# Kernel optimization log

Measured on AMD Instinct MI355X. Metric: run time of the kernel, lower is better.

The kernel has to match this reference:

```python
import jax, jax.numpy as jnp
import numpy as np

BOUND = 1.0          # aabb = [-bound, bound]^3 (aabb_train/aabb_infer)
MIN_NEAR = 0.2
DENSITY_SCALE = 1.0
T_THRESH = 1e-4
BG_COLOR = 1.0
N_RAYS = 262144      # 512x512 image
N_STEPS = 128        # samples per ray


def setup_inputs() -> dict:
    key = jax.random.key(0)
    k1, k2, k3, k4 = jax.random.split(key, 4)
    # ray origins inside the box, unit directions
    rays_o = jax.random.uniform(k1, (N_RAYS, 3), minval=-0.5, maxval=0.5)
    d = jax.random.normal(k2, (N_RAYS, 3))
    rays_d = d / jnp.linalg.norm(d, axis=-1, keepdims=True)
    # per-sample network outputs (the abstract self(xyzs, dirs) call)
    sigmas = jax.random.uniform(k3, (N_RAYS, N_STEPS)) * 10.0
    rgbs = jax.random.uniform(k4, (N_RAYS, N_STEPS, 3))
    return {"rays_o": rays_o, "rays_d": rays_d, "sigmas": sigmas, "rgbs": rgbs}


def reference(rays_o, rays_d, sigmas, rgbs):
    N, S = sigmas.shape
    # --- near_far_from_aabb: slab test against [-BOUND, BOUND]^3 ---
    d = jnp.where(jnp.abs(rays_d) < 1e-8, 1e-8, rays_d)
    t1 = (-BOUND - rays_o) / d                      # [N,3]
    t2 = (BOUND - rays_o) / d                       # [N,3]
    nears = jnp.max(jnp.minimum(t1, t2), axis=-1)   # [N]
    fars = jnp.min(jnp.maximum(t1, t2), axis=-1)    # [N]
    nears = jnp.maximum(nears, MIN_NEAR)
    fars = jnp.maximum(fars, nears + 1e-4)

    # --- uniform marching: per-ray step size ---
    deltas = (fars - nears) / S                     # [N]
    tvals = nears[:, None] + (jnp.arange(S, dtype=sigmas.dtype) + 0.5) * deltas[:, None]  # [N,S]

    # --- composite_rays: alpha compositing with early-termination mask ---
    alphas = 1.0 - jnp.exp(-DENSITY_SCALE * sigmas * deltas[:, None])       # [N,S]
    trans_full = jnp.cumprod(1.0 - alphas + 1e-10, axis=1)                   # [N,S]
    # exclusive transmittance: T_i = prod_{j<i} (1 - alpha_j)
    T = jnp.concatenate([jnp.ones_like(trans_full[:, :1]), trans_full[:, :-1]], axis=1)
    # the CUDA kernel stops marching once T < T_thresh
    weights = alphas * T * (T > T_THRESH).astype(sigmas.dtype)               # [N,S]

    weights_sum = jnp.sum(weights, axis=1)                                   # [N]
    depth = jnp.sum(weights * tvals, axis=1)                                 # [N]
    image = jnp.einsum('ns,nsc->nc', weights, rgbs)                          # [N,3]
    image = image + (1.0 - weights_sum)[:, None] * BG_COLOR
    depth_normalized = jnp.clip(depth - nears, 0.0) / (fars - nears)
    return image, depth, depth_normalized
```

## Files before the change

kernel.cpp:

```cpp
#include <hip/hip_runtime.h>

#define NSTEPS 128
#define MIN_NEAR 0.2f
#define T_THRESH 1e-4f

__global__ __launch_bounds__(256) void nerf_composite(
    const float* __restrict__ rays_o,
    const float* __restrict__ rays_d,
    const float* __restrict__ sigmas,
    const float* __restrict__ rgbs,
    float* __restrict__ out,
    int N)
{
    const int ray  = blockIdx.x * 4 + (threadIdx.x >> 6);
    const int lane = threadIdx.x & 63;
    if (ray >= N) return;

    const float o0 = rays_o[3 * ray + 0];
    const float o1 = rays_o[3 * ray + 1];
    const float o2 = rays_o[3 * ray + 2];
    const float d0 = rays_d[3 * ray + 0];
    const float d1 = rays_d[3 * ray + 1];
    const float d2 = rays_d[3 * ray + 2];

    float tmin = -3.0e38f, tmax = 3.0e38f;
    {
        float dc, ta, tb;
        dc = (fabsf(d0) < 1e-8f) ? 1e-8f : d0;
        ta = (-1.0f - o0) / dc;  tb = (1.0f - o0) / dc;
        tmin = fmaxf(tmin, fminf(ta, tb));  tmax = fminf(tmax, fmaxf(ta, tb));
        dc = (fabsf(d1) < 1e-8f) ? 1e-8f : d1;
        ta = (-1.0f - o1) / dc;  tb = (1.0f - o1) / dc;
        tmin = fmaxf(tmin, fminf(ta, tb));  tmax = fminf(tmax, fmaxf(ta, tb));
        dc = (fabsf(d2) < 1e-8f) ? 1e-8f : d2;
        ta = (-1.0f - o2) / dc;  tb = (1.0f - o2) / dc;
        tmin = fmaxf(tmin, fminf(ta, tb));  tmax = fminf(tmax, fmaxf(ta, tb));
    }
    const float nearv = fmaxf(tmin, MIN_NEAR);
    const float farv  = fmaxf(tmax, nearv + 1e-4f);
    const float delta = (farv - nearv) * (1.0f / (float)NSTEPS);

    const float2* sp = (const float2*)(sigmas + (size_t)ray * NSTEPS);
    const float2 sv = sp[lane];
    const float2* rp = (const float2*)(rgbs + (size_t)ray * NSTEPS * 3);
    const float2 c0 = rp[3 * lane + 0];
    const float2 c1 = rp[3 * lane + 1];
    const float2 c2 = rp[3 * lane + 2];

    const float s0 = sv.x, s1 = sv.y;
    const float r0 = c0.x, g0 = c0.y, b0 = c1.x;
    const float r1 = c1.y, g1 = c2.x, b1 = c2.y;

    const float e0 = __expf(-s0 * delta);
    const float e1 = __expf(-s1 * delta);
    const float a0 = 1.0f - e0;
    const float a1 = 1.0f - e1;
    const float f0 = e0 + 1e-10f;
    const float f1 = e1 + 1e-10f;

    float scan = f0 * f1;
    #pragma unroll
    for (int off = 1; off < 64; off <<= 1) {
        float v = __shfl_up(scan, off, 64);
        if (lane >= off) scan *= v;
    }
    float Texc = __shfl_up(scan, 1, 64);
    if (lane == 0) Texc = 1.0f;
    const float T0 = Texc;
    const float T1 = Texc * f0;

    const float w0 = (T0 > T_THRESH) ? a0 * T0 : 0.0f;
    const float w1 = (T1 > T_THRESH) ? a1 * T1 : 0.0f;

    const float t0 = nearv + ((float)(2 * lane) + 0.5f) * delta;
    const float t1 = nearv + ((float)(2 * lane) + 1.5f) * delta;

    float ws = w0 + w1;
    float dp = w0 * t0 + w1 * t1;
    float ir = w0 * r0 + w1 * r1;
    float ig = w0 * g0 + w1 * g1;
    float ib = w0 * b0 + w1 * b1;

    #pragma unroll
    for (int off = 32; off > 0; off >>= 1) {
        ws += __shfl_xor(ws, off, 64);
        dp += __shfl_xor(dp, off, 64);
        ir += __shfl_xor(ir, off, 64);
        ig += __shfl_xor(ig, off, 64);
        ib += __shfl_xor(ib, off, 64);
    }

    if (lane == 0) {
        const float bg = 1.0f - ws;
        out[3 * ray + 0] = ir + bg;
        out[3 * ray + 1] = ig + bg;
        out[3 * ray + 2] = ib + bg;
        out[3 * N + ray] = dp;
        out[4 * N + ray] = fmaxf(dp - nearv, 0.0f) / (farv - nearv);
    }
}

extern "C" void kernel_launch(void* const* d_in, const int* in_sizes, int n_in,
                              void* d_out, int out_size, void* d_ws, size_t ws_size,
                              hipStream_t stream) {
    const float* rays_o = (const float*)d_in[0];
    const float* rays_d = (const float*)d_in[1];
    const float* sigmas = (const float*)d_in[2];
    const float* rgbs   = (const float*)d_in[3];
    float* out = (float*)d_out;

    const int N = in_sizes[0] / 3;
    const int raysPerBlock = 4;
    const int grid = (N + raysPerBlock - 1) / raysPerBlock;
    nerf_composite<<<grid, 256, 0, stream>>>(rays_o, rays_d, sigmas, rgbs, out, N);
}
```

Baseline: 594.2 us.

## Assign eight lanes per ray with sequential per-lane compositing and float4 loads

Each wavefront now processes eight rays, with eight lanes per ray handling sixteen consecutive samples each. Loads widen to float4, and each lane computes a local transmittance product, then does a three-step segmented scan and reduction instead of six-step wave-wide shuffles. This cuts shuffle and cross-lane overhead and moves more bytes per load. In exchange it uses more registers per thread, which may reduce occupancy, and the per-instruction load strides are less coalesced.

```diff
diff --git a/kernel.cpp b/kernel.cpp
--- a/kernel.cpp
+++ b/kernel.cpp
@@ -12,8 +12,11 @@
     float* __restrict__ out,
     int N)
 {
-    const int ray  = blockIdx.x * 4 + (threadIdx.x >> 6);
+    const int wave = threadIdx.x >> 6;
     const int lane = threadIdx.x & 63;
+    const int seg  = lane >> 3;
+    const int li   = lane & 7;
+    const int ray  = (blockIdx.x * 4 + wave) * 8 + seg;
     if (ray >= N) return;
 
     const float o0 = rays_o[3 * ray + 0];
@@ -22,6 +25,20 @@
     const float d0 = rays_d[3 * ray + 0];
     const float d1 = rays_d[3 * ray + 1];
     const float d2 = rays_d[3 * ray + 2];
+
+    const float4* sp = (const float4*)(sigmas + (size_t)ray * NSTEPS);
+    float4 sv[4];
+    #pragma unroll
+    for (int j = 0; j < 4; ++j) sv[j] = sp[li * 4 + j];
+
+    const float4* rp = (const float4*)(rgbs + (size_t)ray * NSTEPS * 3);
+    float col[48];
+    #pragma unroll
+    for (int j = 0; j < 12; ++j) {
+        float4 c = rp[li * 12 + j];
+        col[4 * j + 0] = c.x; col[4 * j + 1] = c.y;
+        col[4 * j + 2] = c.z; col[4 * j + 3] = c.w;
+    }
 
     float tmin = -3.0e38f, tmax = 3.0e38f;
     {
@@ -40,57 +57,52 @@
     const float farv  = fmaxf(tmax, nearv + 1e-4f);
     const float delta = (farv - nearv) * (1.0f / (float)NSTEPS);
 
-    const float2* sp = (const float2*)(sigmas + (size_t)ray * NSTEPS);
-    const float2 sv = sp[lane];
-    const float2* rp = (const float2*)(rgbs + (size_t)ray * NSTEPS * 3);
-    const float2 c0 = rp[3 * lane + 0];
-    const float2 c1 = rp[3 * lane + 1];
-    const float2 c2 = rp[3 * lane + 2];
+    float e[16];
+    #pragma unroll
+    for (int j = 0; j < 4; ++j) {
+        e[4 * j + 0] = __expf(-sv[j].x * delta);
+        e[4 * j + 1] = __expf(-sv[j].y * delta);
+        e[4 * j + 2] = __expf(-sv[j].z * delta);
+        e[4 * j + 3] = __expf(-sv[j].w * delta);
+    }
+    float P = 1.0f;
+    #pragma unroll
+    for (int k = 0; k < 16; ++k) P *= e[k] + 1e-10f;
 
-    const float s0 = sv.x, s1 = sv.y;
-    const float r0 = c0.x, g0 = c0.y, b0 = c1.x;
-    const float r1 = c1.y, g1 = c2.x, b1 = c2.y;
+    float scan = P;
+    #pragma unroll
+    for (int off = 1; off < 8; off <<= 1) {
+        float v = __shfl_up(scan, off, 8);
+        if (li >= off) scan *= v;
+    }
+    float T = __shfl_up(scan, 1, 8);
+    if (li == 0) T = 1.0f;
 
-    const float e0 = __expf(-s0 * delta);
-    const float e1 = __expf(-s1 * delta);
-    const float a0 = 1.0f - e0;
-    const float a1 = 1.0f - e1;
-    const float f0 = e0 + 1e-10f;
-    const float f1 = e1 + 1e-10f;
-
-    float scan = f0 * f1;
+    const float tbase = nearv + ((float)(li * 16) + 0.5f) * delta;
+    float ws = 0.0f, dp = 0.0f, ir = 0.0f, ig = 0.0f, ib = 0.0f;
     #pragma unroll
-    for (int off = 1; off < 64; off <<= 1) {
-        float v = __shfl_up(scan, off, 64);
-        if (lane >= off) scan *= v;
+    for (int k = 0; k < 16; ++k) {
+        const float a = 1.0f - e[k];
+        const float w = (T > T_THRESH) ? a * T : 0.0f;
+        const float t = tbase + (float)k * delta;
+        ws += w;
+        dp += w * t;
+        ir += w * col[3 * k + 0];
+        ig += w * col[3 * k + 1];
+        ib += w * col[3 * k + 2];
+        T *= e[k] + 1e-10f;
     }
-    float Texc = __shfl_up(scan, 1, 64);
-    if (lane == 0) Texc = 1.0f;
-    const float T0 = Texc;
-    const float T1 = Texc * f0;
-
-    const float w0 = (T0 > T_THRESH) ? a0 * T0 : 0.0f;
-    const float w1 = (T1 > T_THRESH) ? a1 * T1 : 0.0f;
-
-    const float t0 = nearv + ((float)(2 * lane) + 0.5f) * delta;
-    const float t1 = nearv + ((float)(2 * lane) + 1.5f) * delta;
-
-    float ws = w0 + w1;
-    float dp = w0 * t0 + w1 * t1;
-    float ir = w0 * r0 + w1 * r1;
-    float ig = w0 * g0 + w1 * g1;
-    float ib = w0 * b0 + w1 * b1;
 
     #pragma unroll
-    for (int off = 32; off > 0; off >>= 1) {
-        ws += __shfl_xor(ws, off, 64);
-        dp += __shfl_xor(dp, off, 64);
-        ir += __shfl_xor(ir, off, 64);
-        ig += __shfl_xor(ig, off, 64);
-        ib += __shfl_xor(ib, off, 64);
+    for (int off = 4; off > 0; off >>= 1) {
+        ws += __shfl_xor(ws, off, 8);
+        dp += __shfl_xor(dp, off, 8);
+        ir += __shfl_xor(ir, off, 8);
+        ig += __shfl_xor(ig, off, 8);
+        ib += __shfl_xor(ib, off, 8);
     }
 
-    if (lane == 0) {
+    if (li == 0) {
         const float bg = 1.0f - ws;
         out[3 * ray + 0] = ir + bg;
         out[3 * ray + 1] = ig + bg;
@@ -110,7 +122,7 @@
     float* out = (float*)d_out;
 
     const int N = in_sizes[0] / 3;
-    const int raysPerBlock = 4;
+    const int raysPerBlock = 32;
     const int grid = (N + raysPerBlock - 1) / raysPerBlock;
     nerf_composite<<<grid, 256, 0, stream>>>(rays_o, rays_d, sigmas, rgbs, out, N);
 }
```

New measurement: 630.8 us. 1.06x slower.
